# Performance work log

Hardware: AMD Instinct MI355X
Metric: run time of the kernel (lower is better)

## Reference

```python
import jax, jax.numpy as jnp
import numpy as np

N, D, H, E, K = 8192, 1024, 4096, 8, 2


def setup_inputs() -> dict:
    key = jax.random.key(0)
    ks = jax.random.split(key, 4)
    scaled = lambda k, shp, fan: (jax.random.normal(k, shp, jnp.float32) / np.sqrt(fan).astype(np.float32))
    return {
        "x": jax.random.normal(ks[0], (N, D), jnp.float32),
        "Wg": scaled(ks[1], (D, E), D),
        "bg": jnp.zeros((E,), jnp.float32),
        "W1": scaled(ks[2], (E, D, H), D),
        "b1": jnp.zeros((E, H), jnp.float32),
        "W2": scaled(ks[3], (E, H, D), H),
        "b2": jnp.zeros((E, D), jnp.float32),
    }


def reference(x, Wg, bg, W1, b1, W2, b2):
    # Gating: softmax over experts, top-k selection, renormalize top-k probs.
    gate_probs = jax.nn.softmax(x @ Wg + bg, axis=-1)            # [N, E]
    topk_p, topk_i = jax.lax.top_k(gate_probs, K)                # [N, K]
    topk_p = topk_p / topk_p.sum(axis=-1, keepdims=True)
    onehot = jax.nn.one_hot(topk_i, E, dtype=x.dtype)            # [N, K, E]
    # Per-token combine weight for each expert (0 if expert not in top-k).
    w = (onehot * topk_p[..., None]).sum(axis=1)                 # [N, E]

    out = jnp.zeros_like(x)
    for e in range(E):  # fixed small loop over structurally distinct experts
        h = jax.nn.relu(x @ W1[e] + b1[e])                       # dropout = identity (eval)
        out = out + w[:, e:e + 1] * (h @ W2[e] + b2[e])

    # Load-balancing auxiliary loss.
    importance = gate_probs.sum(axis=0)
    importance = importance / importance.sum()
    load = onehot.sum(axis=(0, 1)) / (x.shape[0] * K)            # [E]
    lb_loss = E * (importance * load).sum()
    return out, lb_loss
```

## Files before the change

kernel.cpp:

```cpp
#include <hip/hip_runtime.h>
#include <hip/hip_bf16.h>
#include <math.h>

#define NTOK 8192
#define DDIM 1024
#define HDIM 4096
#define NEXP 8
#define KTOP 2
#define MAXROWS 17408
#define MAXTILES 136

typedef __bf16 bf16x8 __attribute__((ext_vector_type(8)));
typedef float f32x4 __attribute__((ext_vector_type(4)));

#define GAS __attribute__((address_space(1)))
#define LAS __attribute__((address_space(3)))

__device__ __forceinline__ void async16(const void* g, void* l) {
  __builtin_amdgcn_global_load_lds((GAS void*)g, (LAS void*)l, 16, 0, 0);
}

#define XB_OFF     ((size_t)0)
#define W1T_OFF    (XB_OFF + (size_t)NTOK*DDIM*2)
#define ROWOUT_OFF W1T_OFF
#define W2T_OFF    (W1T_OFF + (size_t)NEXP*DDIM*HDIM*2)
#define HB_OFF     (W2T_OFF + (size_t)NEXP*HDIM*DDIM*2)
#define ROWTOK_OFF (HB_OFF + (size_t)MAXROWS*HDIM*2)
#define ROWW_OFF   (ROWTOK_OFF + (size_t)MAXROWS*4)
#define TOKE_OFF   (ROWW_OFF + (size_t)MAXROWS*4)
#define TOKW_OFF   (TOKE_OFF + (size_t)NTOK*KTOP*4)
#define TOKROW_OFF (TOKW_OFF + (size_t)NTOK*KTOP*4)
#define TILEE_OFF  (TOKROW_OFF + (size_t)NTOK*KTOP*4)
#define CNT_OFF    (TILEE_OFF + (size_t)256*4)
#define POS_OFF    (CNT_OFF + 64)
#define IMP_OFF    (POS_OFF + 64)
#define META_OFF   (IMP_OFF + 64)

__global__ void init_kernel(int* counts, float* importance) {
  if (threadIdx.x < NEXP) { counts[threadIdx.x] = 0; importance[threadIdx.x] = 0.f; }
}

__global__ void cast_x_kernel(const float* __restrict__ src, __hip_bfloat16* __restrict__ dst) {
  size_t i = ((size_t)blockIdx.x * blockDim.x + threadIdx.x) * 4;
  if (i < (size_t)NTOK * DDIM) {
    float4 v = *(const float4*)(src + i);
    dst[i + 0] = __float2bfloat16(v.x);
    dst[i + 1] = __float2bfloat16(v.y);
    dst[i + 2] = __float2bfloat16(v.z);
    dst[i + 3] = __float2bfloat16(v.w);
  }
}

__global__ __launch_bounds__(256) void transpose_cast_kernel(
    const float* __restrict__ src, __hip_bfloat16* __restrict__ dst, int R, int C) {
  __shared__ float tile[64][65];
  const int e = blockIdx.z;
  const float* s = src + (size_t)e * R * C;
  __hip_bfloat16* d = dst + (size_t)e * R * C;
  const int c0 = blockIdx.x * 64, r0 = blockIdx.y * 64;
  const int tc = (threadIdx.x & 15) * 4;
  const int tr = threadIdx.x >> 4;
#pragma unroll
  for (int p = 0; p < 4; ++p) {
    float4 v = *(const float4*)&s[(size_t)(r0 + tr + p * 16) * C + c0 + tc];
    tile[tr + p * 16][tc + 0] = v.x;
    tile[tr + p * 16][tc + 1] = v.y;
    tile[tr + p * 16][tc + 2] = v.z;
    tile[tr + p * 16][tc + 3] = v.w;
  }
  __syncthreads();
  const int oc = threadIdx.x >> 4;
  const int orr = (threadIdx.x & 15) * 4;
#pragma unroll
  for (int p = 0; p < 4; ++p) {
    const int c = oc + p * 16;
    __hip_bfloat16 tmp[4];
    tmp[0] = __float2bfloat16(tile[orr + 0][c]);
    tmp[1] = __float2bfloat16(tile[orr + 1][c]);
    tmp[2] = __float2bfloat16(tile[orr + 2][c]);
    tmp[3] = __float2bfloat16(tile[orr + 3][c]);
    *(ushort4*)&d[(size_t)(c0 + c) * R + r0 + orr] = *(ushort4*)tmp;
  }
}

__global__ __launch_bounds__(256) void gating_kernel(
    const float* __restrict__ x, const float* __restrict__ Wg, const float* __restrict__ bg,
    int* __restrict__ tok_e, float* __restrict__ tok_w,
    int* __restrict__ counts, float* __restrict__ importance) {
  const int tid = threadIdx.x, wid = tid >> 6, lane = tid & 63;
  const int t = blockIdx.x * 32 + wid * 8 + (lane >> 3);
  const int e = lane & 7;
  const float* xr = x + (size_t)t * DDIM;
  double dot = 0.0;
  for (int d = 0; d < DDIM; d += 4) {
    float4 xv = *(const float4*)(xr + d);
    dot += (double)xv.x * (double)Wg[(d + 0) * NEXP + e];
    dot += (double)xv.y * (double)Wg[(d + 1) * NEXP + e];
    dot += (double)xv.z * (double)Wg[(d + 2) * NEXP + e];
    dot += (double)xv.w * (double)Wg[(d + 3) * NEXP + e];
  }
  double logit = dot + (double)bg[e];
  double m = logit;
  for (int off = 1; off < 8; off <<= 1) {
    double o = __shfl_xor(m, off, 64);
    m = o > m ? o : m;
  }
  double p = exp(logit - m);
  double s = p;
  for (int off = 1; off < 8; off <<= 1) s += __shfl_xor(s, off, 64);
  float prob = (float)(p / s);

  __shared__ float imp[NEXP];
  __shared__ int cnt[NEXP];
  if (tid < NEXP) { imp[tid] = 0.f; cnt[tid] = 0; }
  __syncthreads();
  atomicAdd(&imp[e], prob);

  float bp = prob; int be = e;
  for (int off = 1; off < 8; off <<= 1) {
    float op = __shfl_xor(bp, off, 64); int oe = __shfl_xor(be, off, 64);
    if (op > bp || (op == bp && oe < be)) { bp = op; be = oe; }
  }
  float p2 = (e == be) ? -1.f : prob;
  float sp = p2; int se = e;
  for (int off = 1; off < 8; off <<= 1) {
    float op = __shfl_xor(sp, off, 64); int oe = __shfl_xor(se, off, 64);
    if (op > sp || (op == sp && oe < se)) { sp = op; se = oe; }
  }
  if (e == 0) {
    float tsum = bp + sp;
    tok_e[t * 2 + 0] = be; tok_e[t * 2 + 1] = se;
    tok_w[t * 2 + 0] = bp / tsum; tok_w[t * 2 + 1] = sp / tsum;
    atomicAdd(&cnt[be], 1); atomicAdd(&cnt[se], 1);
  }
  __syncthreads();
  if (tid < NEXP) {
    atomicAdd(&counts[tid], cnt[tid]);
    atomicAdd(&importance[tid], imp[tid]);
  }
}

__global__ void offsets_kernel(const int* __restrict__ counts, int* pos, int* tile_expert,
                               int* meta, int* row_token) {
  if (threadIdx.x == 0) {
    int pb = 0, tb = 0;
    for (int e = 0; e < NEXP; e++) {
      pos[e] = pb;
      int tiles = (counts[e] + 127) >> 7;
      for (int tt = 0; tt < tiles; ++tt) tile_expert[tb + tt] = e;
      pb += tiles * 128; tb += tiles;
    }
    meta[0] = tb;
  }
  __syncthreads();
  for (int i = threadIdx.x; i < MAXROWS; i += blockDim.x) row_token[i] = -1;
}

__global__ void scatter_kernel(const int* __restrict__ tok_e, const float* __restrict__ tok_w,
                               int* __restrict__ pos, int* __restrict__ row_token,
                               float* __restrict__ row_weight, int* __restrict__ tok_row) {
  __shared__ int lcnt[NEXP], lbase[NEXP];
  const int t = blockIdx.x * 256 + threadIdx.x;
  if (threadIdx.x < NEXP) lcnt[threadIdx.x] = 0;
  __syncthreads();
  const int e0 = tok_e[t * 2 + 0], e1 = tok_e[t * 2 + 1];
  const int s0 = atomicAdd(&lcnt[e0], 1);
  const int s1 = atomicAdd(&lcnt[e1], 1);
  __syncthreads();
  if (threadIdx.x < NEXP) lbase[threadIdx.x] = atomicAdd(&pos[threadIdx.x], lcnt[threadIdx.x]);
  __syncthreads();
  int r0 = lbase[e0] + s0; row_token[r0] = t; row_weight[r0] = tok_w[t * 2 + 0]; tok_row[t * 2 + 0] = r0;
  int r1 = lbase[e1] + s1; row_token[r1] = t; row_weight[r1] = tok_w[t * 2 + 1]; tok_row[t * 2 + 1] = r1;
}

__global__ __launch_bounds__(256) void gemm1_kernel(
    const __hip_bfloat16* __restrict__ xb, const __hip_bfloat16* __restrict__ w1t,
    const float* __restrict__ b1, __hip_bfloat16* __restrict__ hb,
    const int* __restrict__ row_token, const int* __restrict__ tile_expert,
    const int* __restrict__ meta) {
  const int tile_y = blockIdx.y;
  if (tile_y >= meta[0]) return;
  const int n0 = blockIdx.x * 128;
  const int e = tile_expert[tile_y];
  const int r0 = tile_y * 128;
  const int tid = threadIdx.x;
  const int wid = tid >> 6, lane = tid & 63;

  __shared__ __align__(16) __hip_bfloat16 As[4][128 * 32];
  __shared__ __align__(16) __hip_bfloat16 Bs[4][128 * 32];

  const int srow = wid * 32 + (lane >> 2);
  const int g = ((lane & 3) ^ (srow & 3)) * 8;
  int t0 = row_token[r0 + srow];      if (t0 < 0) t0 = 0;
  int t1 = row_token[r0 + srow + 16]; if (t1 < 0) t1 = 0;
  const __hip_bfloat16* ga0 = xb + (size_t)t0 * DDIM + g;
  const __hip_bfloat16* ga1 = xb + (size_t)t1 * DDIM + g;
  const __hip_bfloat16* gb0 = w1t + ((size_t)e * HDIM + n0 + srow) * DDIM + g;
  const __hip_bfloat16* gb1 = gb0 + (size_t)16 * DDIM;
  const int ldsA0 = (wid * 32) * 32, ldsA1 = (wid * 32 + 16) * 32;

  f32x4 acc[4][4] = {};
  const int wm = (wid & 1) * 64, wn = (wid >> 1) * 64;
  const int fr = lane & 15;
  const int soff = ((lane >> 4) ^ (lane & 3)) * 8;
  const int NT = DDIM / 32;

#define STAGE1(b) do { \
    async16(ga0, &As[b][ldsA0]); async16(ga1, &As[b][ldsA1]); \
    async16(gb0, &Bs[b][ldsA0]); async16(gb1, &Bs[b][ldsA1]); } while (0)
#define ADV1 do { ga0 += 32; ga1 += 32; gb0 += 32; gb1 += 32; } while (0)

  STAGE1(0); ADV1;
  STAGE1(1); ADV1;
  for (int kt = 0; kt < NT; ++kt) {
    STAGE1((kt + 2) & 3);
    if (kt + 3 < NT) ADV1;
    asm volatile("s_waitcnt vmcnt(8)" ::: "memory");
    __builtin_amdgcn_s_barrier();
    asm volatile("" ::: "memory");
    __builtin_amdgcn_sched_barrier(0);
    const int cur = kt & 3;
    bf16x8 av[4], bv[4];
#pragma unroll
    for (int i = 0; i < 4; i++) av[i] = *(const bf16x8*)&As[cur][(wm + i * 16 + fr) * 32 + soff];
#pragma unroll
    for (int j = 0; j < 4; j++) bv[j] = *(const bf16x8*)&Bs[cur][(wn + j * 16 + fr) * 32 + soff];
    __builtin_amdgcn_s_setprio(1);
#pragma unroll
    for (int i = 0; i < 4; i++)
#pragma unroll
      for (int j = 0; j < 4; j++)
        acc[i][j] = __builtin_amdgcn_mfma_f32_16x16x32_bf16(av[i], bv[j], acc[i][j], 0, 0, 0);
    __builtin_amdgcn_s_setprio(0);
    __builtin_amdgcn_sched_barrier(0);
  }
#undef STAGE1
#undef ADV1
  asm volatile("s_waitcnt vmcnt(0)" ::: "memory");

  const int crow = (lane >> 4) * 4;
  const int ccol = lane & 15;
#pragma unroll
  for (int j = 0; j < 4; j++) {
    const int gc = n0 + wn + j * 16 + ccol;
    const float bias = b1[e * HDIM + gc];
#pragma unroll
    for (int i = 0; i < 4; i++) {
      const int grb = r0 + wm + i * 16 + crow;
#pragma unroll
      for (int r = 0; r < 4; r++) {
        float v = acc[i][j][r] + bias;
        v = v > 0.f ? v : 0.f;
        hb[(size_t)(grb + r) * HDIM + gc] = __float2bfloat16(v);
      }
    }
  }
}

__global__ __launch_bounds__(256) void gemm2_kernel(
    const __hip_bfloat16* __restrict__ hb, const __hip_bfloat16* __restrict__ w2t,
    const float* __restrict__ b2, __hip_bfloat16* __restrict__ rowout,
    const int* __restrict__ tile_expert, const int* __restrict__ meta) {
  const int tile_y = blockIdx.x % MAXTILES;
  const int cx = blockIdx.x / MAXTILES;
  if (tile_y >= meta[0]) return;
  const int n0 = cx * 128;
  const int e = tile_expert[tile_y];
  const int r0 = tile_y * 128;
  const int tid = threadIdx.x;
  const int wid = tid >> 6, lane = tid & 63;

  __shared__ __align__(16) __hip_bfloat16 As[4][128 * 32];
  __shared__ __align__(16) __hip_bfloat16 Bs[4][128 * 32];

  const int srow = wid * 32 + (lane >> 2);
  const int g = ((lane & 3) ^ (srow & 3)) * 8;
  const __hip_bfloat16* ga0 = hb + ((size_t)r0 + srow) * HDIM + g;
  const __hip_bfloat16* ga1 = ga0 + (size_t)16 * HDIM;
  const __hip_bfloat16* gb0 = w2t + ((size_t)e * DDIM + n0 + srow) * HDIM + g;
  const __hip_bfloat16* gb1 = gb0 + (size_t)16 * HDIM;
  const int ldsA0 = (wid * 32) * 32, ldsA1 = (wid * 32 + 16) * 32;

  f32x4 acc[4][4] = {};
  const int wm = (wid & 1) * 64, wn = (wid >> 1) * 64;
  const int fr = lane & 15;
  const int soff = ((lane >> 4) ^ (lane & 3)) * 8;
  const int NT = HDIM / 32;

#define STAGE2(b) do { \
    async16(ga0, &As[b][ldsA0]); async16(ga1, &As[b][ldsA1]); \
    async16(gb0, &Bs[b][ldsA0]); async16(gb1, &Bs[b][ldsA1]); } while (0)
#define ADV2 do { ga0 += 32; ga1 += 32; gb0 += 32; gb1 += 32; } while (0)

  STAGE2(0); ADV2;
  STAGE2(1); ADV2;
  for (int kt = 0; kt < NT; ++kt) {
    STAGE2((kt + 2) & 3);
    if (kt + 3 < NT) ADV2;
    asm volatile("s_waitcnt vmcnt(8)" ::: "memory");
    __builtin_amdgcn_s_barrier();
    asm volatile("" ::: "memory");
    __builtin_amdgcn_sched_barrier(0);
    const int cur = kt & 3;
    bf16x8 av[4], bv[4];
#pragma unroll
    for (int i = 0; i < 4; i++) av[i] = *(const bf16x8*)&As[cur][(wm + i * 16 + fr) * 32 + soff];
#pragma unroll
    for (int j = 0; j < 4; j++) bv[j] = *(const bf16x8*)&Bs[cur][(wn + j * 16 + fr) * 32 + soff];
    __builtin_amdgcn_s_setprio(1);
#pragma unroll
    for (int i = 0; i < 4; i++)
#pragma unroll
      for (int j = 0; j < 4; j++)
        acc[i][j] = __builtin_amdgcn_mfma_f32_16x16x32_bf16(av[i], bv[j], acc[i][j], 0, 0, 0);
    __builtin_amdgcn_s_setprio(0);
    __builtin_amdgcn_sched_barrier(0);
  }
#undef STAGE2
#undef ADV2
  asm volatile("s_waitcnt vmcnt(0)" ::: "memory");

  const int crow = (lane >> 4) * 4;
  const int ccol = lane & 15;
#pragma unroll
  for (int j = 0; j < 4; j++) {
    const int gc = n0 + wn + j * 16 + ccol;
    const float bias = b2[e * DDIM + gc];
#pragma unroll
    for (int i = 0; i < 4; i++) {
      const int rr = r0 + wm + i * 16 + crow;
#pragma unroll
      for (int r = 0; r < 4; r++)
        rowout[(size_t)(rr + r) * DDIM + gc] = __float2bfloat16(acc[i][j][r] + bias);
    }
  }
}

__global__ __launch_bounds__(256) void combine_kernel(
    const __hip_bfloat16* __restrict__ rowout, const int* __restrict__ tok_row,
    const float* __restrict__ row_weight, float* __restrict__ out) {
  const int idx = blockIdx.x * 256 + threadIdx.x;
  const int t = idx >> 7;
  const int d = (idx & 127) * 8;
  const int r0 = tok_row[t * 2 + 0], r1 = tok_row[t * 2 + 1];
  const float w0 = row_weight[r0], w1 = row_weight[r1];
  bf16x8 a = *(const bf16x8*)&rowout[(size_t)r0 * DDIM + d];
  bf16x8 b = *(const bf16x8*)&rowout[(size_t)r1 * DDIM + d];
  float o[8];
#pragma unroll
  for (int k = 0; k < 8; k++) o[k] = w0 * (float)a[k] + w1 * (float)b[k];
  float* dst = out + (size_t)t * DDIM + d;
  *(float4*)(dst + 0) = make_float4(o[0], o[1], o[2], o[3]);
  *(float4*)(dst + 4) = make_float4(o[4], o[5], o[6], o[7]);
}

__global__ void finalize_kernel(const float* __restrict__ importance,
                                const int* __restrict__ counts, float* __restrict__ lb_out) {
  if (threadIdx.x == 0 && blockIdx.x == 0) {
    float s = 0.f;
    for (int e = 0; e < NEXP; e++) s += importance[e];
    float lb = 0.f;
    for (int e = 0; e < NEXP; e++)
      lb += (importance[e] / s) * ((float)counts[e] / (float)(NTOK * KTOP));
    lb_out[0] = (float)NEXP * lb;
  }
}

extern "C" void kernel_launch(void* const* d_in, const int* in_sizes, int n_in,
                              void* d_out, int out_size, void* d_ws, size_t ws_size,
                              hipStream_t stream) {
  (void)in_sizes; (void)n_in; (void)out_size; (void)ws_size;
  const float* x  = (const float*)d_in[0];
  const float* Wg = (const float*)d_in[1];
  const float* bg = (const float*)d_in[2];
  const float* W1 = (const float*)d_in[3];
  const float* b1 = (const float*)d_in[4];
  const float* W2 = (const float*)d_in[5];
  const float* b2 = (const float*)d_in[6];
  float* out = (float*)d_out;

  char* ws = (char*)d_ws;
  __hip_bfloat16* xb     = (__hip_bfloat16*)(ws + XB_OFF);
  __hip_bfloat16* w1t    = (__hip_bfloat16*)(ws + W1T_OFF);
  __hip_bfloat16* rowout = (__hip_bfloat16*)(ws + ROWOUT_OFF);
  __hip_bfloat16* w2t    = (__hip_bfloat16*)(ws + W2T_OFF);
  __hip_bfloat16* hb     = (__hip_bfloat16*)(ws + HB_OFF);
  int*   row_token  = (int*)(ws + ROWTOK_OFF);
  float* row_weight = (float*)(ws + ROWW_OFF);
  int*   tok_e   = (int*)(ws + TOKE_OFF);
  float* tok_w   = (float*)(ws + TOKW_OFF);
  int*   tok_row = (int*)(ws + TOKROW_OFF);
  int*   tile_e  = (int*)(ws + TILEE_OFF);
  int*   counts  = (int*)(ws + CNT_OFF);
  int*   pos     = (int*)(ws + POS_OFF);
  float* importance = (float*)(ws + IMP_OFF);
  int*   meta    = (int*)(ws + META_OFF);

  init_kernel<<<1, 64, 0, stream>>>(counts, importance);
  cast_x_kernel<<<NTOK * DDIM / 4 / 256, 256, 0, stream>>>(x, xb);
  transpose_cast_kernel<<<dim3(HDIM / 64, DDIM / 64, NEXP), 256, 0, stream>>>(W1, w1t, DDIM, HDIM);
  transpose_cast_kernel<<<dim3(DDIM / 64, HDIM / 64, NEXP), 256, 0, stream>>>(W2, w2t, HDIM, DDIM);
  gating_kernel<<<NTOK / 32, 256, 0, stream>>>(x, Wg, bg, tok_e, tok_w, counts, importance);
  offsets_kernel<<<1, 256, 0, stream>>>(counts, pos, tile_e, meta, row_token);
  scatter_kernel<<<NTOK / 256, 256, 0, stream>>>(tok_e, tok_w, pos, row_token, row_weight, tok_row);
  gemm1_kernel<<<dim3(HDIM / 128, MAXTILES), 256, 0, stream>>>(xb, w1t, b1, hb, row_token, tile_e, meta);
  gemm2_kernel<<<dim3((DDIM / 128) * MAXTILES), 256, 0, stream>>>(hb, w2t, b2, rowout, tile_e, meta);
  combine_kernel<<<NTOK * 128 / 256, 256, 0, stream>>>(rowout, tok_row, row_weight, out);
  finalize_kernel<<<1, 64, 0, stream>>>(importance, counts, out + (size_t)NTOK * DDIM);
}
```

Measured before the change: 874.1 us.

## Unify MoE GEMMs into templated 128x256 tile kernel with 512 threads

Replaces the two separate grouped GEMM kernels with one templated kernel. It uses 128x256 output tiles, 512 threads (8 waves), a K step of 64 with double buffering, and a split-B ping-pong schedule that interleaves B-half loads with MFMA phases. Block indices are remapped across 8 groups (XCD-aware swizzle) to improve L2 locality. The larger tiles raise arithmetic intensity and cut redundant weight and activation loads. The cost is more barriers per iteration, a larger LDS footprint, and more complex wait-count bookkeeping.

```diff
diff --git a/kernel.cpp b/kernel.cpp
--- a/kernel.cpp
+++ b/kernel.cpp
@@ -173,165 +173,139 @@
   int r1 = lbase[e1] + s1; row_token[r1] = t; row_weight[r1] = tok_w[t * 2 + 1]; tok_row[t * 2 + 1] = r1;
 }
 
-__global__ __launch_bounds__(256) void gemm1_kernel(
-    const __hip_bfloat16* __restrict__ xb, const __hip_bfloat16* __restrict__ w1t,
-    const float* __restrict__ b1, __hip_bfloat16* __restrict__ hb,
+template<int NDIM, int KDIM, int NCOLT, bool GATHER, bool RELU>
+__global__ __launch_bounds__(512, 2) void moe_gemm_kernel(
+    const __hip_bfloat16* __restrict__ Ag, const __hip_bfloat16* __restrict__ Bg,
+    const float* __restrict__ bias, __hip_bfloat16* __restrict__ Cg,
     const int* __restrict__ row_token, const int* __restrict__ tile_expert,
     const int* __restrict__ meta) {
-  const int tile_y = blockIdx.y;
-  if (tile_y >= meta[0]) return;
-  const int n0 = blockIdx.x * 128;
-  const int e = tile_expert[tile_y];
-  const int r0 = tile_y * 128;
-  const int tid = threadIdx.x;
-  const int wid = tid >> 6, lane = tid & 63;
-
-  __shared__ __align__(16) __hip_bfloat16 As[4][128 * 32];
-  __shared__ __align__(16) __hip_bfloat16 Bs[4][128 * 32];
-
-  const int srow = wid * 32 + (lane >> 2);
-  const int g = ((lane & 3) ^ (srow & 3)) * 8;
-  int t0 = row_token[r0 + srow];      if (t0 < 0) t0 = 0;
-  int t1 = row_token[r0 + srow + 16]; if (t1 < 0) t1 = 0;
-  const __hip_bfloat16* ga0 = xb + (size_t)t0 * DDIM + g;
-  const __hip_bfloat16* ga1 = xb + (size_t)t1 * DDIM + g;
-  const __hip_bfloat16* gb0 = w1t + ((size_t)e * HDIM + n0 + srow) * DDIM + g;
-  const __hip_bfloat16* gb1 = gb0 + (size_t)16 * DDIM;
-  const int ldsA0 = (wid * 32) * 32, ldsA1 = (wid * 32 + 16) * 32;
+  const int id = blockIdx.x;
+  const int v = (id & 7) * ((int)gridDim.x >> 3) + (id >> 3);
+  const int ty = v / NCOLT, cx = v % NCOLT;
+  if (ty >= meta[0]) return;
+  const int e = tile_expert[ty];
+  const int r0 = ty * 128;
+  const int n0 = cx * 256;
+  const int tid = threadIdx.x, wid = tid >> 6, lane = tid & 63;
+  const int wm = wid >> 2, wn = wid & 3;
+  const int fr = lane & 15;
+  const int NT = KDIM / 64;
+
+  __shared__ __align__(16) __hip_bfloat16 Al[2][128][64];
+  __shared__ __align__(16) __hip_bfloat16 Bl[2][256][64];
+
+  const int l8 = lane >> 3;
+  const int gsrc = (lane & 7) ^ l8;
+  const __hip_bfloat16* aptr[2];
+  const __hip_bfloat16* bptr0[2];
+  const __hip_bfloat16* bptr1[2];
+#pragma unroll
+  for (int i = 0; i < 2; ++i) {
+    const int c = wid * 2 + i;
+    const int arow = r0 + c * 8 + l8;
+    if (GATHER) {
+      int t = row_token[arow]; if (t < 0) t = 0;
+      aptr[i] = Ag + (size_t)t * KDIM + gsrc * 8;
+    } else {
+      aptr[i] = Ag + (size_t)arow * KDIM + gsrc * 8;
+    }
+    bptr0[i] = Bg + ((size_t)e * NDIM + n0 + c * 8 + l8) * KDIM + gsrc * 8;
+    bptr1[i] = bptr0[i] + (size_t)128 * KDIM;
+  }
+
+#define ST_A(buf, kk)  do { _Pragma("unroll") for (int i = 0; i < 2; ++i) \
+    async16(aptr[i]  + (kk) * 64, &Al[buf][(wid * 2 + i) * 8][0]); } while (0)
+#define ST_B0(buf, kk) do { _Pragma("unroll") for (int i = 0; i < 2; ++i) \
+    async16(bptr0[i] + (kk) * 64, &Bl[buf][(wid * 2 + i) * 8][0]); } while (0)
+#define ST_B1(buf, kk) do { _Pragma("unroll") for (int i = 0; i < 2; ++i) \
+    async16(bptr1[i] + (kk) * 64, &Bl[buf][128 + (wid * 2 + i) * 8][0]); } while (0)
+
+  const int g4 = lane >> 4, r7 = lane & 7;
+  const int s0e = ((0 + g4) ^ r7) * 8;
+  const int s1e = ((4 + g4) ^ r7) * 8;
 
   f32x4 acc[4][4] = {};
-  const int wm = (wid & 1) * 64, wn = (wid >> 1) * 64;
-  const int fr = lane & 15;
-  const int soff = ((lane >> 4) ^ (lane & 3)) * 8;
-  const int NT = DDIM / 32;
-
-#define STAGE1(b) do { \
-    async16(ga0, &As[b][ldsA0]); async16(ga1, &As[b][ldsA1]); \
-    async16(gb0, &Bs[b][ldsA0]); async16(gb1, &Bs[b][ldsA1]); } while (0)
-#define ADV1 do { ga0 += 32; ga1 += 32; gb0 += 32; gb1 += 32; } while (0)
-
-  STAGE1(0); ADV1;
-  STAGE1(1); ADV1;
+
+  ST_A(0, 0); ST_B0(0, 0); ST_B1(0, 0);
+  ST_A(1, 1); ST_B0(1, 1);
+  asm volatile("s_waitcnt vmcnt(6)" ::: "memory");
+  __builtin_amdgcn_sched_barrier(0);
+  __builtin_amdgcn_s_barrier();
+
+#pragma unroll 1
   for (int kt = 0; kt < NT; ++kt) {
-    STAGE1((kt + 2) & 3);
-    if (kt + 3 < NT) ADV1;
-    asm volatile("s_waitcnt vmcnt(8)" ::: "memory");
+    const int cur = kt & 1, nxt = cur ^ 1;
+    const int kk1 = (kt + 1 < NT) ? kt + 1 : NT - 1;
+    const int kk2 = (kt + 2 < NT) ? kt + 2 : NT - 1;
+    bf16x8 av[4][2], bv[2][2];
+#pragma unroll
+    for (int mi = 0; mi < 4; ++mi) {
+      av[mi][0] = *(const bf16x8*)&Al[cur][wm * 64 + mi * 16 + fr][s0e];
+      av[mi][1] = *(const bf16x8*)&Al[cur][wm * 64 + mi * 16 + fr][s1e];
+    }
+#pragma unroll
+    for (int j = 0; j < 2; ++j) {
+      bv[j][0] = *(const bf16x8*)&Bl[cur][wn * 32 + j * 16 + fr][s0e];
+      bv[j][1] = *(const bf16x8*)&Bl[cur][wn * 32 + j * 16 + fr][s1e];
+    }
+    ST_B1(nxt, kk1);
     __builtin_amdgcn_s_barrier();
-    asm volatile("" ::: "memory");
+    asm volatile("s_waitcnt lgkmcnt(0)" ::: "memory");
     __builtin_amdgcn_sched_barrier(0);
-    const int cur = kt & 3;
-    bf16x8 av[4], bv[4];
-#pragma unroll
-    for (int i = 0; i < 4; i++) av[i] = *(const bf16x8*)&As[cur][(wm + i * 16 + fr) * 32 + soff];
-#pragma unroll
-    for (int j = 0; j < 4; j++) bv[j] = *(const bf16x8*)&Bs[cur][(wn + j * 16 + fr) * 32 + soff];
     __builtin_amdgcn_s_setprio(1);
 #pragma unroll
-    for (int i = 0; i < 4; i++)
-#pragma unroll
-      for (int j = 0; j < 4; j++)
-        acc[i][j] = __builtin_amdgcn_mfma_f32_16x16x32_bf16(av[i], bv[j], acc[i][j], 0, 0, 0);
+    for (int mi = 0; mi < 4; ++mi)
+#pragma unroll
+      for (int j = 0; j < 2; ++j)
+#pragma unroll
+        for (int k = 0; k < 2; ++k)
+          acc[mi][j] = __builtin_amdgcn_mfma_f32_16x16x32_bf16(av[mi][k], bv[j][k], acc[mi][j], 0, 0, 0);
     __builtin_amdgcn_s_setprio(0);
+    asm volatile("s_waitcnt vmcnt(6)" ::: "memory");
     __builtin_amdgcn_sched_barrier(0);
-  }
-#undef STAGE1
-#undef ADV1
+    __builtin_amdgcn_s_barrier();
+#pragma unroll
+    for (int j = 0; j < 2; ++j) {
+      bv[j][0] = *(const bf16x8*)&Bl[cur][128 + wn * 32 + j * 16 + fr][s0e];
+      bv[j][1] = *(const bf16x8*)&Bl[cur][128 + wn * 32 + j * 16 + fr][s1e];
+    }
+    ST_A(cur, kk2); ST_B0(cur, kk2);
+    __builtin_amdgcn_s_barrier();
+    asm volatile("s_waitcnt lgkmcnt(0)" ::: "memory");
+    __builtin_amdgcn_sched_barrier(0);
+    __builtin_amdgcn_s_setprio(1);
+#pragma unroll
+    for (int mi = 0; mi < 4; ++mi)
+#pragma unroll
+      for (int j = 0; j < 2; ++j)
+#pragma unroll
+        for (int k = 0; k < 2; ++k)
+          acc[mi][2 + j] = __builtin_amdgcn_mfma_f32_16x16x32_bf16(av[mi][k], bv[j][k], acc[mi][2 + j], 0, 0, 0);
+    __builtin_amdgcn_s_setprio(0);
+    asm volatile("s_waitcnt vmcnt(6)" ::: "memory");
+    __builtin_amdgcn_sched_barrier(0);
+    __builtin_amdgcn_s_barrier();
+  }
+#undef ST_A
+#undef ST_B0
+#undef ST_B1
   asm volatile("s_waitcnt vmcnt(0)" ::: "memory");
 
   const int crow = (lane >> 4) * 4;
   const int ccol = lane & 15;
 #pragma unroll
-  for (int j = 0; j < 4; j++) {
-    const int gc = n0 + wn + j * 16 + ccol;
-    const float bias = b1[e * HDIM + gc];
-#pragma unroll
-    for (int i = 0; i < 4; i++) {
-      const int grb = r0 + wm + i * 16 + crow;
-#pragma unroll
-      for (int r = 0; r < 4; r++) {
-        float v = acc[i][j][r] + bias;
-        v = v > 0.f ? v : 0.f;
-        hb[(size_t)(grb + r) * HDIM + gc] = __float2bfloat16(v);
+  for (int nj = 0; nj < 4; ++nj) {
+    const int gc = n0 + (nj >> 1) * 128 + wn * 32 + (nj & 1) * 16 + ccol;
+    const float bv_ = bias[e * NDIM + gc];
+#pragma unroll
+    for (int mi = 0; mi < 4; ++mi) {
+      const int grb = r0 + wm * 64 + mi * 16 + crow;
+#pragma unroll
+      for (int r = 0; r < 4; ++r) {
+        float vv = acc[mi][nj][r] + bv_;
+        if (RELU) vv = vv > 0.f ? vv : 0.f;
+        Cg[(size_t)(grb + r) * NDIM + gc] = __float2bfloat16(vv);
       }
-    }
-  }
-}
-
-__global__ __launch_bounds__(256) void gemm2_kernel(
-    const __hip_bfloat16* __restrict__ hb, const __hip_bfloat16* __restrict__ w2t,
-    const float* __restrict__ b2, __hip_bfloat16* __restrict__ rowout,
-    const int* __restrict__ tile_expert, const int* __restrict__ meta) {
-  const int tile_y = blockIdx.x % MAXTILES;
-  const int cx = blockIdx.x / MAXTILES;
-  if (tile_y >= meta[0]) return;
-  const int n0 = cx * 128;
-  const int e = tile_expert[tile_y];
-  const int r0 = tile_y * 128;
-  const int tid = threadIdx.x;
-  const int wid = tid >> 6, lane = tid & 63;
-
-  __shared__ __align__(16) __hip_bfloat16 As[4][128 * 32];
-  __shared__ __align__(16) __hip_bfloat16 Bs[4][128 * 32];
-
-  const int srow = wid * 32 + (lane >> 2);
-  const int g = ((lane & 3) ^ (srow & 3)) * 8;
-  const __hip_bfloat16* ga0 = hb + ((size_t)r0 + srow) * HDIM + g;
-  const __hip_bfloat16* ga1 = ga0 + (size_t)16 * HDIM;
-  const __hip_bfloat16* gb0 = w2t + ((size_t)e * DDIM + n0 + srow) * HDIM + g;
-  const __hip_bfloat16* gb1 = gb0 + (size_t)16 * HDIM;
-  const int ldsA0 = (wid * 32) * 32, ldsA1 = (wid * 32 + 16) * 32;
-
-  f32x4 acc[4][4] = {};
-  const int wm = (wid & 1) * 64, wn = (wid >> 1) * 64;
-  const int fr = lane & 15;
-  const int soff = ((lane >> 4) ^ (lane & 3)) * 8;
-  const int NT = HDIM / 32;
-
-#define STAGE2(b) do { \
-    async16(ga0, &As[b][ldsA0]); async16(ga1, &As[b][ldsA1]); \
-    async16(gb0, &Bs[b][ldsA0]); async16(gb1, &Bs[b][ldsA1]); } while (0)
-#define ADV2 do { ga0 += 32; ga1 += 32; gb0 += 32; gb1 += 32; } while (0)
-
-  STAGE2(0); ADV2;
-  STAGE2(1); ADV2;
-  for (int kt = 0; kt < NT; ++kt) {
-    STAGE2((kt + 2) & 3);
-    if (kt + 3 < NT) ADV2;
-    asm volatile("s_waitcnt vmcnt(8)" ::: "memory");
-    __builtin_amdgcn_s_barrier();
-    asm volatile("" ::: "memory");
-    __builtin_amdgcn_sched_barrier(0);
-    const int cur = kt & 3;
-    bf16x8 av[4], bv[4];
-#pragma unroll
-    for (int i = 0; i < 4; i++) av[i] = *(const bf16x8*)&As[cur][(wm + i * 16 + fr) * 32 + soff];
-#pragma unroll
-    for (int j = 0; j < 4; j++) bv[j] = *(const bf16x8*)&Bs[cur][(wn + j * 16 + fr) * 32 + soff];
-    __builtin_amdgcn_s_setprio(1);
-#pragma unroll
-    for (int i = 0; i < 4; i++)
-#pragma unroll
-      for (int j = 0; j < 4; j++)
-        acc[i][j] = __builtin_amdgcn_mfma_f32_16x16x32_bf16(av[i], bv[j], acc[i][j], 0, 0, 0);
-    __builtin_amdgcn_s_setprio(0);
-    __builtin_amdgcn_sched_barrier(0);
-  }
-#undef STAGE2
-#undef ADV2
-  asm volatile("s_waitcnt vmcnt(0)" ::: "memory");
-
-  const int crow = (lane >> 4) * 4;
-  const int ccol = lane & 15;
-#pragma unroll
-  for (int j = 0; j < 4; j++) {
-    const int gc = n0 + wn + j * 16 + ccol;
-    const float bias = b2[e * DDIM + gc];
-#pragma unroll
-    for (int i = 0; i < 4; i++) {
-      const int rr = r0 + wm + i * 16 + crow;
-#pragma unroll
-      for (int r = 0; r < 4; r++)
-        rowout[(size_t)(rr + r) * DDIM + gc] = __float2bfloat16(acc[i][j][r] + bias);
     }
   }
 }
@@ -403,8 +377,10 @@
   gating_kernel<<<NTOK / 32, 256, 0, stream>>>(x, Wg, bg, tok_e, tok_w, counts, importance);
   offsets_kernel<<<1, 256, 0, stream>>>(counts, pos, tile_e, meta, row_token);
   scatter_kernel<<<NTOK / 256, 256, 0, stream>>>(tok_e, tok_w, pos, row_token, row_weight, tok_row);
-  gemm1_kernel<<<dim3(HDIM / 128, MAXTILES), 256, 0, stream>>>(xb, w1t, b1, hb, row_token, tile_e, meta);
-  gemm2_kernel<<<dim3((DDIM / 128) * MAXTILES), 256, 0, stream>>>(hb, w2t, b2, rowout, tile_e, meta);
+  moe_gemm_kernel<HDIM, DDIM, HDIM / 256, true, true>
+      <<<MAXTILES * (HDIM / 256), 512, 0, stream>>>(xb, w1t, b1, hb, row_token, tile_e, meta);
+  moe_gemm_kernel<DDIM, HDIM, DDIM / 256, false, false>
+      <<<MAXTILES * (DDIM / 256), 512, 0, stream>>>(hb, w2t, b2, rowout, row_token, tile_e, meta);
   combine_kernel<<<NTOK * 128 / 256, 256, 0, stream>>>(rowout, tok_row, row_weight, out);
   finalize_kernel<<<1, 64, 0, stream>>>(importance, counts, out + (size_t)NTOK * DDIM);
 }
```

Result: faster. 839.1 us (-4.0%).
